# Kernel tuning notes

Hardware: AMD Instinct MI355X
Metric: run time of the kernel (lower is better)

The kernel has to match this reference:

```python
import jax, jax.numpy as jnp
import numpy as np

B, H, W, C = 32, 64, 64, 512
NUM_HEADS = 16
WS = 8          # window_size
SHIFT = 4       # shift_size = WS // 2
MLP_HIDDEN = 2048
N = WS * WS     # tokens per window
NW = (H // WS) * (W // WS)  # windows per image


def _rel_coords_table():
    # Swin-V2 log-spaced continuous relative coordinates, (1, 2*WS-1, 2*WS-1, 2)
    r = np.arange(-(WS - 1), WS, dtype=np.float32)
    t = np.stack(np.meshgrid(r, r, indexing='ij'), axis=-1)[None]
    t = t / (WS - 1) * 8.0
    t = np.sign(t) * np.log2(np.abs(t) + 1.0) / np.log2(8.0)
    return t.astype(np.float32)


def _rel_pos_index():
    coords = np.stack(np.meshgrid(np.arange(WS), np.arange(WS), indexing='ij'))
    cf = coords.reshape(2, -1)
    rel = (cf[:, :, None] - cf[:, None, :]).transpose(1, 2, 0)
    rel[..., 0] += WS - 1
    rel[..., 1] += WS - 1
    rel[..., 0] *= 2 * WS - 1
    return rel.sum(-1)  # (N, N) int


def _attn_mask():
    # shifted-window mask: -100 where tokens come from different image regions
    img = np.zeros((H, W), np.float32)
    cnt = 0
    for hs in (slice(0, -WS), slice(-WS, -SHIFT), slice(-SHIFT, None)):
        for ws_ in (slice(0, -WS), slice(-WS, -SHIFT), slice(-SHIFT, None)):
            img[hs, ws_] = cnt
            cnt += 1
    mw = img.reshape(H // WS, WS, W // WS, WS).transpose(0, 2, 1, 3).reshape(-1, N)
    diff = mw[:, None, :] - mw[:, :, None]
    return np.where(diff != 0, np.float32(-100.0), np.float32(0.0))  # (NW, N, N)


_RCT = jnp.asarray(_rel_coords_table())
_RPI = jnp.asarray(_rel_pos_index().reshape(-1))
_MASK = jnp.asarray(_attn_mask())
_LOGIT_MAX = float(np.log(1.0 / 0.01))


def _layernorm(x, w, b):
    mu = x.mean(-1, keepdims=True)
    var = ((x - mu) ** 2).mean(-1, keepdims=True)
    return (x - mu) / jnp.sqrt(var + 1e-5) * w + b


def setup_inputs() -> dict:
    key = jax.random.key(0)
    ks = jax.random.split(key, 8)
    s = 0.02
    return {
        'x': jax.random.normal(ks[0], (B, H * W, C), jnp.float32),
        'qkv_w': jax.random.normal(ks[1], (3 * C, C), jnp.float32) * s,
        'q_bias': jnp.zeros((C,), jnp.float32),
        'v_bias': jnp.zeros((C,), jnp.float32),
        'logit_scale': jnp.log(10.0 * jnp.ones((NUM_HEADS, 1, 1), jnp.float32)),
        'cpb_w1': jax.random.normal(ks[2], (512, 2), jnp.float32) * s,
        'cpb_b1': jnp.zeros((512,), jnp.float32),
        'cpb_w2': jax.random.normal(ks[3], (NUM_HEADS, 512), jnp.float32) * s,
        'proj_w': jax.random.normal(ks[4], (C, C), jnp.float32) * s,
        'proj_b': jnp.zeros((C,), jnp.float32),
        'norm1_w': jnp.ones((C,), jnp.float32),
        'norm1_b': jnp.zeros((C,), jnp.float32),
        'norm2_w': jnp.ones((C,), jnp.float32),
        'norm2_b': jnp.zeros((C,), jnp.float32),
        'fc1_w': jax.random.normal(ks[5], (MLP_HIDDEN, C), jnp.float32) * s,
        'fc1_b': jnp.zeros((MLP_HIDDEN,), jnp.float32),
        'fc2_w': jax.random.normal(ks[6], (C, MLP_HIDDEN), jnp.float32) * s,
        'fc2_b': jnp.zeros((C,), jnp.float32),
    }


def reference(x, qkv_w, q_bias, v_bias, logit_scale, cpb_w1, cpb_b1, cpb_w2,
              proj_w, proj_b, norm1_w, norm1_b, norm2_w, norm2_b,
              fc1_w, fc1_b, fc2_w, fc2_b):
    hd = C // NUM_HEADS
    shortcut = x
    xi = x.reshape(B, H, W, C)
    xi = jnp.roll(xi, shift=(-SHIFT, -SHIFT), axis=(1, 2))
    # window partition -> (B*NW, N, C)
    xw = xi.reshape(B, H // WS, WS, W // WS, WS, C).transpose(0, 1, 3, 2, 4, 5).reshape(-1, N, C)
    # qkv with q/v bias only (k bias = 0), Swin-V2 style
    qkv_b = jnp.concatenate([q_bias, jnp.zeros_like(v_bias), v_bias])
    qkv = (xw @ qkv_w.T + qkv_b).reshape(-1, N, 3, NUM_HEADS, hd).transpose(2, 0, 3, 1, 4)
    q, k, v = qkv[0], qkv[1], qkv[2]  # (B_, nH, N, hd)
    # cosine attention
    qn = q / jnp.maximum(jnp.linalg.norm(q, axis=-1, keepdims=True), 1e-12)
    kn = k / jnp.maximum(jnp.linalg.norm(k, axis=-1, keepdims=True), 1e-12)
    attn = jnp.einsum('whnd,whmd->whnm', qn, kn)
    scale = jnp.exp(jnp.minimum(logit_scale, _LOGIT_MAX))  # (nH,1,1)
    attn = attn * scale
    # continuous relative position bias via small MLP
    table = (jax.nn.relu(_RCT @ cpb_w1.T + cpb_b1) @ cpb_w2.T).reshape(-1, NUM_HEADS)
    bias = table[_RPI].reshape(N, N, NUM_HEADS).transpose(2, 0, 1)  # (nH, N, N)
    bias = 16.0 * jax.nn.sigmoid(bias)
    attn = attn + bias[None]
    # shift mask
    attn = attn.reshape(B, NW, NUM_HEADS, N, N) + _MASK[None, :, None]
    attn = jax.nn.softmax(attn.reshape(-1, NUM_HEADS, N, N), axis=-1)
    out = jnp.einsum('whnm,whmd->whnd', attn, v).transpose(0, 2, 1, 3).reshape(-1, N, C)
    out = out @ proj_w.T + proj_b
    # window reverse + un-shift
    xi = out.reshape(B, H // WS, W // WS, WS, WS, C).transpose(0, 1, 3, 2, 4, 5).reshape(B, H, W, C)
    xi = jnp.roll(xi, shift=(SHIFT, SHIFT), axis=(1, 2)).reshape(B, H * W, C)
    # Swin-V2 post-norm residuals
    x = shortcut + _layernorm(xi, norm1_w, norm1_b)
    h = jax.nn.gelu(x @ fc1_w.T + fc1_b, approximate=False)
    y = h @ fc2_w.T + fc2_b
    x = x + _layernorm(y, norm2_w, norm2_b)
    return x
```

## Files before the change

### kernel.cpp

```cpp
#include <hip/hip_runtime.h>

typedef unsigned short u16;
typedef unsigned int u32;
typedef __attribute__((ext_vector_type(8))) __bf16 bf16x8;
typedef __attribute__((ext_vector_type(8))) short s16x8;
typedef __attribute__((ext_vector_type(4))) short s16x4;
typedef __attribute__((ext_vector_type(4))) float f32x4;

static __device__ __forceinline__ float bf2f(u16 h){
  union{u32 u; float f;} v; v.u = ((u32)h)<<16; return v.f;
}
static __device__ __forceinline__ u16 f2bf(float f){
  union{float f; u32 u;} v; v.f = f; u32 u = v.u;
  return (u16)((u + 0x7fffu + ((u>>16)&1u)) >> 16);
}
static __device__ __forceinline__ u16 cvtbf(float f){
  return __builtin_bit_cast(u16, (__bf16)f);
}

#define GLD16(gp, lp) __builtin_amdgcn_global_load_lds(                      \
  (__attribute__((address_space(1))) void*)(void*)(gp),                      \
  (__attribute__((address_space(3))) void*)(void*)(lp), 16, 0, 0)

__global__ __launch_bounds__(256)
void prep_x_kernel(const float* __restrict__ x, u16* __restrict__ xw)
{
  const int t = threadIdx.x, wv = t>>6, ln = t&63;
  const size_t row = (size_t)blockIdx.x*4 + wv;
  const int b = (int)(row>>12), wl = (int)((row>>6)&63), m = (int)(row&63);
  const int gh = ((wl>>3)*8 + (m>>3) + 4) & 63;
  const int gw = ((wl&7)*8 + (m&7) + 4) & 63;
  const size_t src = ((size_t)b*4096 + (size_t)gh*64 + gw)*512 + (size_t)ln*8;
  f32x4 a = *(const f32x4*)&x[src];
  f32x4 c = *(const f32x4*)&x[src+4];
  s16x8 o;
#pragma unroll
  for (int j=0;j<4;j++){ o[j] = (short)cvtbf(a[j]); o[j+4] = (short)cvtbf(c[j]); }
  *(s16x8*)&xw[row*512 + (size_t)ln*8] = o;
}

__global__ __launch_bounds__(256)
void cvt_bf16_kernel(const float* __restrict__ src, u16* __restrict__ dst, int n)
{
  const int i = (blockIdx.x*256 + threadIdx.x)*8;
  if (i >= n) return;
  f32x4 a = *(const f32x4*)&src[i];
  f32x4 c = *(const f32x4*)&src[i+4];
  s16x8 o;
#pragma unroll
  for (int j=0;j<4;j++){ o[j] = (short)cvtbf(a[j]); o[j+4] = (short)cvtbf(c[j]); }
  *(s16x8*)&dst[i] = o;
}

static __device__ __forceinline__ float logcoord(int d){
  const float tt = (float)d * (8.0f/7.0f);
  const float sg = (tt > 0.f) ? 1.f : ((tt < 0.f) ? -1.f : 0.f);
  return sg * log2f(fabsf(tt) + 1.f) * (1.f/3.f);
}

__global__ __launch_bounds__(512)
void cpb_table_kernel(const float* __restrict__ w1, const float* __restrict__ b1,
                      const float* __restrict__ w2, float* __restrict__ table)
{
  __shared__ float hid[512];
  const int r = blockIdx.x, j = threadIdx.x;
  const float va = logcoord(r/15 - 7);
  const float vb = logcoord(r%15 - 7);
  hid[j] = fmaxf(va*w1[2*j] + vb*w1[2*j+1] + b1[j], 0.f);
  __syncthreads();
  if (j < 16){
    float acc = 0.f;
    for (int i=0;i<512;i++) acc += hid[i]*w2[j*512+i];
    table[r*16 + j] = acc;
  }
}

__global__ __launch_bounds__(256)
void bias_expand_kernel(const float* __restrict__ table, float* __restrict__ biasT)
{
  const int gid = blockIdx.x*256 + threadIdx.x;
  const int h = gid>>12, ij = gid&4095, i = ij>>6, j = ij&63;
  const int dr = (i>>3)-(j>>3)+7, dc = (i&7)-(j&7)+7;
  const float v = table[(dr*15+dc)*16 + h];
  biasT[gid] = 16.f / (1.f + __expf(-v));
}

template<int EPI>
__global__ __launch_bounds__(256)
void gemm_bt(const u16* __restrict__ A, const u16* __restrict__ B,
             u16* __restrict__ Co, const float* __restrict__ bias0,
             const float* __restrict__ bias1, int N, int K)
{
  __shared__ u16 ls[2][2][128*32];
  const int t = threadIdx.x;
  const int wv = t>>6, ln = t&63;
  const int wr = wv>>1, wc = wv&1;
  const int lr = ln&15, lg = ln>>4;
  const int gx = gridDim.x;
  const int lin = blockIdx.y*gx + blockIdx.x;
  const int q = (gx*gridDim.y)>>3;
  const int lin2 = (lin&7)*q + (lin>>3);
  const int mT = lin2/gx, nT = lin2 - mT*gx;

  const int rsub = ln>>2;
  const int csub = (ln&3)*8;
  const u16* ga0 = A + ((size_t)(mT*128 + wv*16 + rsub))*K + csub;
  const u16* gb0 = B + ((size_t)(nT*128 + wv*16 + rsub))*K + csub;

#define STAGE_K(buf, k0) do {                                                \
  _Pragma("unroll")                                                          \
  for (int i_=0;i_<2;i_++){                                                  \
    GLD16(ga0 + (size_t)i_*64*K + (k0), (char*)(&ls[buf][0][0]) + i_*4096 + wv*1024); \
    GLD16(gb0 + (size_t)i_*64*K + (k0), (char*)(&ls[buf][1][0]) + i_*4096 + wv*1024); \
  }                                                                          \
} while(0)

  f32x4 acc[4][4] = {};
  const int nsteps = K>>5;
  STAGE_K(0, 0);
  __syncthreads();
#pragma unroll 2
  for (int tt = 0; tt < nsteps; ++tt) {
    const int cur = tt&1;
    if (tt+1 < nsteps) STAGE_K(cur^1, (tt+1)*32);
    const u16* la = &ls[cur][0][0];
    const u16* lb = &ls[cur][1][0];
    bf16x8 af[4], bfv[4];
#pragma unroll
    for (int mt=0;mt<4;mt++)
      af[mt] = *(const bf16x8*)&la[(wr*64 + mt*16 + lr)*32 + lg*8];
#pragma unroll
    for (int nt=0;nt<4;nt++)
      bfv[nt] = *(const bf16x8*)&lb[(wc*64 + nt*16 + lr)*32 + lg*8];
#pragma unroll
    for (int mt=0;mt<4;mt++)
#pragma unroll
      for (int nt=0;nt<4;nt++)
        acc[mt][nt] = __builtin_amdgcn_mfma_f32_16x16x32_bf16(af[mt], bfv[nt], acc[mt][nt], 0,0,0);
    __syncthreads();
  }
#undef STAGE_K

  if (EPI == 0) {
    const int c0 = nT*128 + wc*64;
    const int sec = c0 >> 9;
    const int wrow = mT*2 + wr;
    const float* bsrc = (sec==0) ? bias0 : bias1;
#pragma unroll
    for (int nt=0; nt<4; nt++) {
      const int hh = ((c0 + nt*16) >> 5) & 15;
      const int d  = ((nt&1)<<4) + lr;
      const float bb = (sec==1) ? 0.f : bsrc[(hh<<5)+d];
      u16* p = Co + ((size_t)(sec*32768 + wrow*16 + hh))*2048 + d;
#pragma unroll
      for (int mt=0; mt<4; mt++) {
        u16* pm = p + (mt*16 + lg*4)*32;
#pragma unroll
        for (int rr=0; rr<4; rr++)
          pm[rr*32] = cvtbf(acc[mt][nt][rr] + bb);
      }
    }
  } else {
    const int c0 = nT*128 + wc*64;
    const int r0 = mT*128 + wr*64 + lg*4;
#pragma unroll
    for (int nt=0; nt<4; nt++) {
      const int col = c0 + nt*16 + lr;
      const float bb = bias0[col];
#pragma unroll
      for (int mt=0; mt<4; mt++) {
        u16* pm = Co + (size_t)(r0 + mt*16)*N + col;
#pragma unroll
        for (int rr=0; rr<4; rr++) {
          float v = acc[mt][nt][rr] + bb;
          if (EPI == 2) {
            const float z = 1.5957691216f * v * fmaf(0.044715f, v*v, 1.0f);
            v = v * __builtin_amdgcn_rcpf(1.0f + __expf(-z));
          }
          pm[rr*N] = cvtbf(v);
        }
      }
    }
  }
}

__global__ __launch_bounds__(256)
void attn_win(const u16* __restrict__ qkv, const float* __restrict__ biasT,
              const float* __restrict__ logit_scale, u16* __restrict__ aout)
{
  __shared__ float sb[4096];
  __shared__ u16 sp[4][4096];
  __shared__ u16 svt[4][2048];
  const int t = threadIdx.x, wv = t>>6, ln = t&63;
  const int lr = ln&15, lg = ln>>4;
  const int head = blockIdx.y;
  for (int i = t; i < 4096; i += 256) sb[i] = biasT[head*4096 + i];
  __syncthreads();
  const int win = blockIdx.x*4 + wv;
  const size_t whi = (size_t)win*16 + head;
  const u16* qb = qkv + whi*2048;
  const u16* kb = qkv + 67108864ULL + whi*2048;
  const u16* vb = qkv + 134217728ULL + whi*2048;

  s16x8 qs[4], ks[4];
  float qin[4], kin[4];
#pragma unroll
  for (int mt=0;mt<4;mt++){
    qs[mt] = *(const s16x8*)&qb[(mt*16+lr)*32 + lg*8];
    float ss = 0.f;
#pragma unroll
    for (int j=0;j<8;j++){ float f = bf2f((u16)qs[mt][j]); ss += f*f; }
    ss += __shfl_xor(ss, 16); ss += __shfl_xor(ss, 32);
    qin[mt] = 1.f / fmaxf(sqrtf(ss), 1e-12f);
  }
#pragma unroll
  for (int nt=0;nt<4;nt++){
    ks[nt] = *(const s16x8*)&kb[(nt*16+lr)*32 + lg*8];
    float ss = 0.f;
#pragma unroll
    for (int j=0;j<8;j++){ float f = bf2f((u16)ks[nt][j]); ss += f*f; }
    ss += __shfl_xor(ss, 16); ss += __shfl_xor(ss, 32);
    kin[nt] = 1.f / fmaxf(sqrtf(ss), 1e-12f);
  }
  f32x4 S[4][4] = {};
#pragma unroll
  for (int mt=0;mt<4;mt++)
#pragma unroll
    for (int nt=0;nt<4;nt++)
      S[mt][nt] = __builtin_amdgcn_mfma_f32_16x16x32_bf16(
          __builtin_bit_cast(bf16x8, qs[mt]), __builtin_bit_cast(bf16x8, ks[nt]),
          S[mt][nt], 0,0,0);

  const float scale = expf(fminf(logit_scale[head], 4.6051702f));
  const int wl = win & 63, wh = wl>>3, ww = wl&7;
  float rsum[4][4];
#pragma unroll
  for (int mt=0;mt<4;mt++){
#pragma unroll
    for (int rr=0;rr<4;rr++){
      const int msub = lg*4 + rr;
      const float qn = __shfl(qin[mt], msub);
      const int m = mt*16 + msub;
      const int ridm = (wh==7 ? (((m>>3)<4) ? 3 : 6) : 0) + (ww==7 ? (((m&7)<4) ? 1 : 2) : 0);
#pragma unroll
      for (int nt=0;nt<4;nt++){
        const int n = nt*16 + lr;
        const int ridn = (wh==7 ? (((n>>3)<4) ? 3 : 6) : 0) + (ww==7 ? (((n&7)<4) ? 1 : 2) : 0);
        float v = S[mt][nt][rr] * (qn * kin[nt] * scale) + sb[m*64+n];
        if (ridm != ridn) v -= 100.f;
        S[mt][nt][rr] = v;
      }
      float mx = fmaxf(fmaxf(S[mt][0][rr], S[mt][1][rr]), fmaxf(S[mt][2][rr], S[mt][3][rr]));
      mx = fmaxf(mx, __shfl_xor(mx, 1)); mx = fmaxf(mx, __shfl_xor(mx, 2));
      mx = fmaxf(mx, __shfl_xor(mx, 4)); mx = fmaxf(mx, __shfl_xor(mx, 8));
      float sm = 0.f;
#pragma unroll
      for (int nt=0;nt<4;nt++){ float p = __expf(S[mt][nt][rr]-mx); S[mt][nt][rr] = p; sm += p; }
      sm += __shfl_xor(sm,1); sm += __shfl_xor(sm,2); sm += __shfl_xor(sm,4); sm += __shfl_xor(sm,8);
      rsum[mt][rr] = sm;
#pragma unroll
      for (int nt=0;nt<4;nt++){
        const int n = nt*16 + lr;
        sp[wv][(m*64 + n) ^ ((m&7)<<3)] = cvtbf(S[mt][nt][rr]);
      }
    }
  }
#pragma unroll
  for (int it=0; it<8; it++){
    const int flat = it*256 + ln*4;
    const int k = flat>>5, d0 = flat&31;
    s16x4 vv = *(const s16x4*)&vb[k*32 + d0];
#pragma unroll
    for (int e=0;e<4;e++)
      svt[wv][((d0+e)*64 + k) ^ (((d0+e)&7)<<3)] = (u16)vv[e];
  }
  f32x4 O[4][2] = {};
#pragma unroll
  for (int kk=0; kk<2; kk++){
    bf16x8 pf[4], vf[2];
#pragma unroll
    for (int mt=0;mt<4;mt++){
      const int am = mt*16 + lr;
      const int idx = (am*64 + kk*32 + lg*8) ^ ((am&7)<<3);
      s16x8 tmp; __builtin_memcpy(&tmp, (const char*)&sp[wv][0] + 2*idx, 16);
      pf[mt] = __builtin_bit_cast(bf16x8, tmp);
    }
#pragma unroll
    for (int n2=0;n2<2;n2++){
      const int vn = n2*16 + lr;
      const int idx = (vn*64 + kk*32 + lg*8) ^ ((vn&7)<<3);
      s16x8 tmp; __builtin_memcpy(&tmp, (const char*)&svt[wv][0] + 2*idx, 16);
      vf[n2] = __builtin_bit_cast(bf16x8, tmp);
    }
#pragma unroll
    for (int mt=0;mt<4;mt++)
#pragma unroll
      for (int n2=0;n2<2;n2++)
        O[mt][n2] = __builtin_amdgcn_mfma_f32_16x16x32_bf16(pf[mt], vf[n2], O[mt][n2], 0,0,0);
  }
  const size_t obase = (size_t)win*64;
#pragma unroll
  for (int mt=0;mt<4;mt++)
#pragma unroll
  for (int rr=0;rr<4;rr++){
    const int m = mt*16 + lg*4 + rr;
    const float inv = 1.f / rsum[mt][rr];
#pragma unroll
    for (int n2=0;n2<2;n2++){
      const int d = n2*16 + lr;
      aout[(obase + m)*512 + head*32 + d] = cvtbf(O[mt][n2][rr] * inv);
    }
  }
}

__global__ __launch_bounds__(256)
void scatter_ln_kernel(const u16* __restrict__ po, const float* __restrict__ x,
                       const float* __restrict__ w, const float* __restrict__ bb,
                       float* __restrict__ x1f, u16* __restrict__ x1b)
{
  const int t = threadIdx.x, wv = t>>6, ln = t&63;
  const size_t row = (size_t)blockIdx.x*4 + wv;
  s16x8 pv = *(const s16x8*)&po[row*512 + (size_t)ln*8];
  float v[8]; float s=0.f, s2=0.f;
#pragma unroll
  for (int j=0;j<8;j++){ v[j] = bf2f((u16)pv[j]); s += v[j]; s2 += v[j]*v[j]; }
#pragma unroll
  for (int d=1; d<64; d<<=1){ s += __shfl_xor(s,d); s2 += __shfl_xor(s2,d); }
  const float mu = s * 0.001953125f;
  const float var = s2 * 0.001953125f - mu*mu;
  const float rs = rsqrtf(var + 1e-5f);
  const int b = (int)(row>>12), wl = (int)((row>>6)&63), m = (int)(row&63);
  const int gh = ((wl>>3)*8 + (m>>3) + 4) & 63;
  const int gw = ((wl&7)*8 + (m&7) + 4) & 63;
  const size_t img = ((size_t)b*4096 + (size_t)gh*64 + gw)*512 + (size_t)ln*8;
  f32x4 xa = *(const f32x4*)&x[img];
  f32x4 xc = *(const f32x4*)&x[img+4];
  f32x4 oa, oc; s16x8 ob;
  const int c0 = ln*8;
#pragma unroll
  for (int j=0;j<8;j++){
    const int c = c0 + j;
    const float lnv = (v[j]-mu)*rs*w[c] + bb[c];
    const float xx = (j<4) ? xa[j] : xc[j-4];
    const float o = xx + lnv;
    if (j<4) oa[j] = o; else oc[j-4] = o;
    ob[j] = (short)cvtbf(o);
  }
  *(f32x4*)&x1f[img] = oa;
  *(f32x4*)&x1f[img+4] = oc;
  *(s16x8*)&x1b[img] = ob;
}

__global__ __launch_bounds__(256)
void final_ln_kernel(const u16* __restrict__ y, const float* __restrict__ w,
                     const float* __restrict__ bb, float* __restrict__ out)
{
  const int t = threadIdx.x, wv = t>>6, ln = t&63;
  const size_t row = (size_t)blockIdx.x*4 + wv;
  s16x8 yv = *(const s16x8*)&y[row*512 + (size_t)ln*8];
  float v[8]; float s=0.f, s2=0.f;
#pragma unroll
  for (int j=0;j<8;j++){ v[j] = bf2f((u16)yv[j]); s += v[j]; s2 += v[j]*v[j]; }
#pragma unroll
  for (int d=1; d<64; d<<=1){ s += __shfl_xor(s,d); s2 += __shfl_xor(s2,d); }
  const float mu = s * 0.001953125f;
  const float var = s2 * 0.001953125f - mu*mu;
  const float rs = rsqrtf(var + 1e-5f);
  const size_t idx = row*512 + (size_t)ln*8;
  f32x4 xa = *(const f32x4*)&out[idx];
  f32x4 xc = *(const f32x4*)&out[idx+4];
  f32x4 oa, oc;
  const int c0 = ln*8;
#pragma unroll
  for (int j=0;j<8;j++){
    const int c = c0 + j;
    const float lnv = (v[j]-mu)*rs*w[c] + bb[c];
    const float xx = (j<4) ? xa[j] : xc[j-4];
    if (j<4) oa[j] = xx + lnv; else oc[j-4] = xx + lnv;
  }
  *(f32x4*)&out[idx] = oa;
  *(f32x4*)&out[idx+4] = oc;
}

extern "C" void kernel_launch(void* const* d_in, const int* in_sizes, int n_in,
                              void* d_out, int out_size, void* d_ws, size_t ws_size,
                              hipStream_t stream)
{
  (void)in_sizes; (void)n_in; (void)out_size; (void)ws_size;
  const float* x        = (const float*)d_in[0];
  const float* qkv_w    = (const float*)d_in[1];
  const float* q_bias   = (const float*)d_in[2];
  const float* v_bias   = (const float*)d_in[3];
  const float* lscale   = (const float*)d_in[4];
  const float* cpb_w1   = (const float*)d_in[5];
  const float* cpb_b1   = (const float*)d_in[6];
  const float* cpb_w2   = (const float*)d_in[7];
  const float* proj_w   = (const float*)d_in[8];
  const float* proj_b   = (const float*)d_in[9];
  const float* n1w      = (const float*)d_in[10];
  const float* n1b      = (const float*)d_in[11];
  const float* n2w      = (const float*)d_in[12];
  const float* n2b      = (const float*)d_in[13];
  const float* fc1_w    = (const float*)d_in[14];
  const float* fc1_b    = (const float*)d_in[15];
  const float* fc2_w    = (const float*)d_in[16];
  const float* fc2_b    = (const float*)d_in[17];

  char* ws = (char*)d_ws;
  constexpr size_t XW_OFF   = 0;
  constexpr size_t ATT_OFF  = 134217728ULL;
  constexpr size_t PRJ_OFF  = 268435456ULL;
  constexpr size_t H_OFF    = 0;
  constexpr size_t BIAS_OFF = 536870912ULL;
  constexpr size_t TAB_OFF  = BIAS_OFF + 262144;
  constexpr size_t WQKV_OFF = TAB_OFF + 16384;
  constexpr size_t WPRJ_OFF = WQKV_OFF + 1572864;
  constexpr size_t WFC1_OFF = WPRJ_OFF + 524288;
  constexpr size_t WFC2_OFF = WFC1_OFF + 2097152;
  constexpr size_t QKV_OFF  = WFC2_OFF + 2097152;
  constexpr size_t X1B_OFF  = QKV_OFF;
  constexpr size_t Y_OFF    = QKV_OFF + 134217728ULL;

  u16*   xw    = (u16*)(ws + XW_OFF);
  u16*   attnO = (u16*)(ws + ATT_OFF);
  u16*   projO = (u16*)(ws + PRJ_OFF);
  u16*   hbuf  = (u16*)(ws + H_OFF);
  float* biasT = (float*)(ws + BIAS_OFF);
  float* table = (float*)(ws + TAB_OFF);
  u16*   wqkv  = (u16*)(ws + WQKV_OFF);
  u16*   wprj  = (u16*)(ws + WPRJ_OFF);
  u16*   wfc1  = (u16*)(ws + WFC1_OFF);
  u16*   wfc2  = (u16*)(ws + WFC2_OFF);
  u16*   qkvB  = (u16*)(ws + QKV_OFF);
  u16*   x1b   = (u16*)(ws + X1B_OFF);
  u16*   ybuf  = (u16*)(ws + Y_OFF);
  float* x1f   = (float*)d_out;

  cvt_bf16_kernel<<<384, 256, 0, stream>>>(qkv_w, wqkv, 786432);
  cvt_bf16_kernel<<<128, 256, 0, stream>>>(proj_w, wprj, 262144);
  cvt_bf16_kernel<<<512, 256, 0, stream>>>(fc1_w, wfc1, 1048576);
  cvt_bf16_kernel<<<512, 256, 0, stream>>>(fc2_w, wfc2, 1048576);
  prep_x_kernel<<<32768, 256, 0, stream>>>(x, xw);
  cpb_table_kernel<<<225, 512, 0, stream>>>(cpb_w1, cpb_b1, cpb_w2, table);
  bias_expand_kernel<<<256, 256, 0, stream>>>(table, biasT);
  gemm_bt<0><<<dim3(12,1024), 256, 0, stream>>>(xw, wqkv, qkvB, q_bias, v_bias, 1536, 512);
  attn_win<<<dim3(512,16), 256, 0, stream>>>(qkvB, biasT, lscale, attnO);
  gemm_bt<1><<<dim3(4,1024), 256, 0, stream>>>(attnO, wprj, projO, proj_b, nullptr, 512, 512);
  scatter_ln_kernel<<<32768, 256, 0, stream>>>(projO, x, n1w, n1b, x1f, x1b);
  gemm_bt<2><<<dim3(16,1024), 256, 0, stream>>>(x1b, wfc1, hbuf, fc1_b, nullptr, 2048, 512);
  gemm_bt<3><<<dim3(4,1024), 256, 0, stream>>>(hbuf, wfc2, ybuf, fc2_b, nullptr, 512, 2048);
  final_ln_kernel<<<32768, 256, 0, stream>>>(ybuf, n2w, n2b, (float*)d_out);
}
```

Baseline: 1.843 ms.

## Replace 128x128 GEMM with 256x256-tile, 4-stage pipelined, swizzled-LDS GEMM

Every projection and MLP GEMM now uses 256x256 output tiles computed by 512 threads (8 waves, each owning 128x64). Operands are staged into a 4-deep ring of dynamic LDS buffers (128 KB) through direct global-to-LDS loads with an XOR swizzle that avoids bank conflicts. Waits use explicit vmcnt counts so loads stay two steps ahead of compute, and MFMA sections are bracketed with s_setprio. This is meant to raise data reuse per load and hide memory latency, at the cost of one block per CU and a larger register footprint from 32 accumulators per wave.

```diff
diff --git a/kernel.cpp b/kernel.cpp
--- a/kernel.cpp
+++ b/kernel.cpp
@@ -9,10 +9,6 @@
 
 static __device__ __forceinline__ float bf2f(u16 h){
   union{u32 u; float f;} v; v.u = ((u32)h)<<16; return v.f;
-}
-static __device__ __forceinline__ u16 f2bf(float f){
-  union{float f; u32 u;} v; v.f = f; u32 u = v.u;
-  return (u16)((u + 0x7fffu + ((u>>16)&1u)) >> 16);
 }
 static __device__ __forceinline__ u16 cvtbf(float f){
   return __builtin_bit_cast(u16, (__bf16)f);
@@ -86,89 +82,104 @@
 }
 
 template<int EPI>
-__global__ __launch_bounds__(256)
-void gemm_bt(const u16* __restrict__ A, const u16* __restrict__ B,
+__global__ __launch_bounds__(512)
+void gemm256(const u16* __restrict__ A, const u16* __restrict__ B,
              u16* __restrict__ Co, const float* __restrict__ bias0,
              const float* __restrict__ bias1, int N, int K)
 {
-  __shared__ u16 ls[2][2][128*32];
+  extern __shared__ u16 ls[];
   const int t = threadIdx.x;
   const int wv = t>>6, ln = t&63;
-  const int wr = wv>>1, wc = wv&1;
+  const int wr = wv>>2, wc = wv&3;
   const int lr = ln&15, lg = ln>>4;
   const int gx = gridDim.x;
   const int lin = blockIdx.y*gx + blockIdx.x;
-  const int q = (gx*gridDim.y)>>3;
+  const int q = (gx*(int)gridDim.y)>>3;
   const int lin2 = (lin&7)*q + (lin>>3);
   const int mT = lin2/gx, nT = lin2 - mT*gx;
 
-  const int rsub = ln>>2;
-  const int csub = (ln&3)*8;
-  const u16* ga0 = A + ((size_t)(mT*128 + wv*16 + rsub))*K + csub;
-  const u16* gb0 = B + ((size_t)(nT*128 + wv*16 + rsub))*K + csub;
-
-#define STAGE_K(buf, k0) do {                                                \
-  _Pragma("unroll")                                                          \
-  for (int i_=0;i_<2;i_++){                                                  \
-    GLD16(ga0 + (size_t)i_*64*K + (k0), (char*)(&ls[buf][0][0]) + i_*4096 + wv*1024); \
-    GLD16(gb0 + (size_t)i_*64*K + (k0), (char*)(&ls[buf][1][0]) + i_*4096 + wv*1024); \
-  }                                                                          \
-} while(0)
-
-  f32x4 acc[4][4] = {};
+  const int rS = wv*32 + (ln>>2);
+  const int cS = ((ln&3) ^ ((ln>>3)&3)) * 8;
+  const u16* gA0 = A + (size_t)(mT*256 + rS)*K + cS;
+  const u16* gB0 = B + (size_t)(nT*256 + rS)*K + cS;
+  const size_t rstep = (size_t)16*K;
+  char* lW = (char*)ls + wv*2048;
+
+  const int cR = (lg ^ ((lr>>1)&3))*8;
+  const int offA0 = (wr*128 + lr)*32 + cR;
+  const int offB0 = (wc*64  + lr)*32 + cR;
+
+#define STAGE(tt) do {                                                       \
+    char* lb_ = lW + ((tt)&3)*32768;                                         \
+    const size_t ko_ = (size_t)(tt)*32;                                      \
+    GLD16(gA0 + ko_,         lb_);                                           \
+    GLD16(gA0 + ko_ + rstep, lb_ + 1024);                                    \
+    GLD16(gB0 + ko_,         lb_ + 16384);                                   \
+    GLD16(gB0 + ko_ + rstep, lb_ + 16384 + 1024);                            \
+  } while(0)
+
+  f32x4 acc[8][4] = {};
+
+#define COMPUTE(tt) do {                                                     \
+    const u16* la_ = ls + ((tt)&3)*16384;                                    \
+    const u16* lb2_ = la_ + 8192;                                            \
+    bf16x8 bfr[4];                                                           \
+    _Pragma("unroll")                                                        \
+    for (int nt=0;nt<4;nt++) bfr[nt] = *(const bf16x8*)&lb2_[offB0 + nt*512];\
+    __builtin_amdgcn_s_setprio(1);                                           \
+    _Pragma("unroll")                                                        \
+    for (int mt=0;mt<8;mt++){                                                \
+      bf16x8 af = *(const bf16x8*)&la_[offA0 + mt*512];                      \
+      _Pragma("unroll")                                                      \
+      for (int nt=0;nt<4;nt++)                                               \
+        acc[mt][nt] = __builtin_amdgcn_mfma_f32_16x16x32_bf16(af, bfr[nt], acc[mt][nt], 0,0,0); \
+    }                                                                        \
+    __builtin_amdgcn_s_setprio(0);                                           \
+  } while(0)
+
   const int nsteps = K>>5;
-  STAGE_K(0, 0);
-  __syncthreads();
-#pragma unroll 2
-  for (int tt = 0; tt < nsteps; ++tt) {
-    const int cur = tt&1;
-    if (tt+1 < nsteps) STAGE_K(cur^1, (tt+1)*32);
-    const u16* la = &ls[cur][0][0];
-    const u16* lb = &ls[cur][1][0];
-    bf16x8 af[4], bfv[4];
-#pragma unroll
-    for (int mt=0;mt<4;mt++)
-      af[mt] = *(const bf16x8*)&la[(wr*64 + mt*16 + lr)*32 + lg*8];
-#pragma unroll
-    for (int nt=0;nt<4;nt++)
-      bfv[nt] = *(const bf16x8*)&lb[(wc*64 + nt*16 + lr)*32 + lg*8];
-#pragma unroll
-    for (int mt=0;mt<4;mt++)
-#pragma unroll
-      for (int nt=0;nt<4;nt++)
-        acc[mt][nt] = __builtin_amdgcn_mfma_f32_16x16x32_bf16(af[mt], bfv[nt], acc[mt][nt], 0,0,0);
-    __syncthreads();
-  }
-#undef STAGE_K
+  STAGE(0); STAGE(1);
+  for (int t_=0; t_<nsteps-2; ++t_){
+    STAGE(t_+2);
+    asm volatile("s_waitcnt vmcnt(8)\n\ts_barrier" ::: "memory");
+    COMPUTE(t_);
+  }
+  asm volatile("s_waitcnt vmcnt(4)\n\ts_barrier" ::: "memory");
+  COMPUTE(nsteps-2);
+  asm volatile("s_waitcnt vmcnt(0)\n\ts_barrier" ::: "memory");
+  COMPUTE(nsteps-1);
+#undef STAGE
+#undef COMPUTE
 
   if (EPI == 0) {
-    const int c0 = nT*128 + wc*64;
-    const int sec = c0 >> 9;
-    const int wrow = mT*2 + wr;
-    const float* bsrc = (sec==0) ? bias0 : bias1;
+    const int cb0 = nT*256 + wc*64;
 #pragma unroll
     for (int nt=0; nt<4; nt++) {
-      const int hh = ((c0 + nt*16) >> 5) & 15;
-      const int d  = ((nt&1)<<4) + lr;
-      const float bb = (sec==1) ? 0.f : bsrc[(hh<<5)+d];
-      u16* p = Co + ((size_t)(sec*32768 + wrow*16 + hh))*2048 + d;
-#pragma unroll
-      for (int mt=0; mt<4; mt++) {
-        u16* pm = p + (mt*16 + lg*4)*32;
+      const int cb  = cb0 + nt*16;
+      const int sec = cb >> 9;
+      const int hh  = (cb >> 5) & 15;
+      const int d   = (cb & 16) + lr;
+      const float bb = (sec==1) ? 0.f : ((sec==0)?bias0:bias1)[(hh<<5)+d];
+      u16* base = Co + ((size_t)sec*32768 + hh)*2048 + d;
+#pragma unroll
+      for (int mt=0; mt<8; mt++) {
+        const int row = mT*256 + wr*128 + mt*16 + lg*4;
+        const int win = row>>6, tok0 = row&63;
+        u16* p = base + (size_t)win*32768 + tok0*32;
 #pragma unroll
         for (int rr=0; rr<4; rr++)
-          pm[rr*32] = cvtbf(acc[mt][nt][rr] + bb);
+          p[rr*32] = cvtbf(acc[mt][nt][rr] + bb);
       }
     }
   } else {
-    const int c0 = nT*128 + wc*64;
-    const int r0 = mT*128 + wr*64 + lg*4;
+    const int c0 = nT*256 + wc*64;
+    const int r0 = mT*256 + wr*128 + lg*4;
 #pragma unroll
     for (int nt=0; nt<4; nt++) {
       const int col = c0 + nt*16 + lr;
       const float bb = bias0[col];
 #pragma unroll
-      for (int mt=0; mt<4; mt++) {
+      for (int mt=0; mt<8; mt++) {
         u16* pm = Co + (size_t)(r0 + mt*16)*N + col;
 #pragma unroll
         for (int rr=0; rr<4; rr++) {
@@ -436,6 +447,11 @@
   u16*   ybuf  = (u16*)(ws + Y_OFF);
   float* x1f   = (float*)d_out;
 
+  hipFuncSetAttribute((const void*)gemm256<0>, hipFuncAttributeMaxDynamicSharedMemorySize, 131072);
+  hipFuncSetAttribute((const void*)gemm256<1>, hipFuncAttributeMaxDynamicSharedMemorySize, 131072);
+  hipFuncSetAttribute((const void*)gemm256<2>, hipFuncAttributeMaxDynamicSharedMemorySize, 131072);
+  hipFuncSetAttribute((const void*)gemm256<3>, hipFuncAttributeMaxDynamicSharedMemorySize, 131072);
+
   cvt_bf16_kernel<<<384, 256, 0, stream>>>(qkv_w, wqkv, 786432);
   cvt_bf16_kernel<<<128, 256, 0, stream>>>(proj_w, wprj, 262144);
   cvt_bf16_kernel<<<512, 256, 0, stream>>>(fc1_w, wfc1, 1048576);
@@ -443,11 +459,11 @@
   prep_x_kernel<<<32768, 256, 0, stream>>>(x, xw);
   cpb_table_kernel<<<225, 512, 0, stream>>>(cpb_w1, cpb_b1, cpb_w2, table);
   bias_expand_kernel<<<256, 256, 0, stream>>>(table, biasT);
-  gemm_bt<0><<<dim3(12,1024), 256, 0, stream>>>(xw, wqkv, qkvB, q_bias, v_bias, 1536, 512);
+  gemm256<0><<<dim3(6,512), 512, 131072, stream>>>(xw, wqkv, qkvB, q_bias, v_bias, 1536, 512);
   attn_win<<<dim3(512,16), 256, 0, stream>>>(qkvB, biasT, lscale, attnO);
-  gemm_bt<1><<<dim3(4,1024), 256, 0, stream>>>(attnO, wprj, projO, proj_b, nullptr, 512, 512);
+  gemm256<1><<<dim3(2,512), 512, 131072, stream>>>(attnO, wprj, projO, proj_b, nullptr, 512, 512);
   scatter_ln_kernel<<<32768, 256, 0, stream>>>(projO, x, n1w, n1b, x1f, x1b);
-  gemm_bt<2><<<dim3(16,1024), 256, 0, stream>>>(x1b, wfc1, hbuf, fc1_b, nullptr, 2048, 512);
-  gemm_bt<3><<<dim3(4,1024), 256, 0, stream>>>(hbuf, wfc2, ybuf, fc2_b, nullptr, 512, 2048);
+  gemm256<2><<<dim3(8,512), 512, 131072, stream>>>(x1b, wfc1, hbuf, fc1_b, nullptr, 2048, 512);
+  gemm256<3><<<dim3(2,512), 512, 131072, stream>>>(hbuf, wfc2, ybuf, fc2_b, nullptr, 512, 2048);
   final_ln_kernel<<<32768, 256, 0, stream>>>(ybuf, n2w, n2b, (float*)d_out);
 }
```

Result: faster. 1.742 ms (-5.5%).
